# Kernel optimization log

Hardware: AMD Instinct MI355X
Metric: run time of the kernel (lower is better)

Reference implementation:

```python
import jax, jax.numpy as jnp
import numpy as np

B, S, D = 2, 2048, 2048
N_HEADS, N_KV_HEADS, HEAD_DIM = 16, 8, 128
N_REP = N_HEADS // N_KV_HEADS
EPS = 1e-6
SCALE = HEAD_DIM ** -0.5


def setup_inputs() -> dict:
    key = jax.random.key(0)
    ks = jax.random.split(key, 6)
    x = jax.random.normal(ks[0], (B, S, D), dtype=jnp.float32)
    # RoPE frequencies (Llama-style cis stored as interleaved [cos, sin])
    inv_freq = 1.0 / (1e6 ** (jnp.arange(0, HEAD_DIM, 2, dtype=jnp.float32) / HEAD_DIM))
    angles = jnp.arange(S, dtype=jnp.float32)[:, None] * inv_freq[None, :]  # [S, HEAD_DIM//2]
    freqs_cis = jnp.stack([jnp.cos(angles), jnp.sin(angles)], axis=-1)  # [S, HEAD_DIM//2, 2]
    wq = jax.random.normal(ks[1], (N_HEADS * HEAD_DIM, D), dtype=jnp.float32) * 0.02
    wk = jax.random.normal(ks[2], (N_KV_HEADS * HEAD_DIM, D), dtype=jnp.float32) * 0.02
    wv = jax.random.normal(ks[3], (N_KV_HEADS * HEAD_DIM, D), dtype=jnp.float32) * 0.02
    wo = jax.random.normal(ks[4], (D, N_HEADS * HEAD_DIM), dtype=jnp.float32) * 0.02
    q_norm_w = jnp.ones((HEAD_DIM,), dtype=jnp.float32)
    k_norm_w = jnp.ones((HEAD_DIM,), dtype=jnp.float32)
    return {"x": x, "freqs_cis": freqs_cis, "wq": wq, "wk": wk, "wv": wv,
            "wo": wo, "q_norm_w": q_norm_w, "k_norm_w": k_norm_w}


def _rmsnorm(t, w):
    var = jnp.mean(jnp.square(t), axis=-1, keepdims=True)
    return t * jax.lax.rsqrt(var + EPS) * w


def _apply_rope(t, cos, sin):
    # t: [B, S, H, HEAD_DIM]; cos/sin: [1, S, 1, HEAD_DIM//2]
    tp = t.reshape(*t.shape[:-1], HEAD_DIM // 2, 2)
    tr, ti = tp[..., 0], tp[..., 1]
    out = jnp.stack([tr * cos - ti * sin, tr * sin + ti * cos], axis=-1)
    return out.reshape(t.shape)


def reference(x, freqs_cis, wq, wk, wv, wo, q_norm_w, k_norm_w):
    bs, seqlen, _ = x.shape
    xq = (x @ wq.T).reshape(bs, seqlen, N_HEADS, HEAD_DIM)
    xk = (x @ wk.T).reshape(bs, seqlen, N_KV_HEADS, HEAD_DIM)
    xv = (x @ wv.T).reshape(bs, seqlen, N_KV_HEADS, HEAD_DIM)
    # per-head RMSNorm (Qwen3)
    xq = _rmsnorm(xq, q_norm_w)
    xk = _rmsnorm(xk, k_norm_w)
    # rotary embedding
    cos = freqs_cis[:seqlen, :, 0][None, :, None, :]
    sin = freqs_cis[:seqlen, :, 1][None, :, None, :]
    xq = _apply_rope(xq, cos, sin)
    xk = _apply_rope(xk, cos, sin)
    # GQA: repeat kv heads
    keys = jnp.repeat(xk, N_REP, axis=2)    # [B, S, N_HEADS, HEAD_DIM]
    values = jnp.repeat(xv, N_REP, axis=2)
    q = xq.transpose(0, 2, 1, 3)   # [B, H, S, D]
    k = keys.transpose(0, 2, 1, 3)
    v = values.transpose(0, 2, 1, 3)
    scores = jnp.einsum("bhqd,bhkd->bhqk", q, k) * SCALE
    causal = jnp.tril(jnp.ones((seqlen, seqlen), dtype=bool))
    scores = jnp.where(causal[None, None], scores, jnp.finfo(scores.dtype).min)
    attn = jax.nn.softmax(scores, axis=-1)
    out = jnp.einsum("bhqk,bhkd->bhqd", attn, v)
    out = out.transpose(0, 2, 1, 3).reshape(bs, seqlen, N_HEADS * HEAD_DIM)
    return out @ wo.T
```

## Files before the change

kernel.cpp:

```cpp
#include <hip/hip_runtime.h>

#define B_ 2
#define S_ 2048
#define D_ 2048
#define NH 16
#define NKV 8
#define HD 128
#define SCALE 0.08838834764831845f
#define CEXP 0.1275255f
#define RTHR 62.733f

typedef unsigned short u16;
typedef __attribute__((ext_vector_type(8))) short short8;
typedef __attribute__((ext_vector_type(4))) float f32x4;
typedef __attribute__((ext_vector_type(16))) float f32x16;
typedef __attribute__((ext_vector_type(4))) int i32x4;
typedef __attribute__((ext_vector_type(2))) int i32x2;

#define ASM_VMCNT(N) asm volatile("s_waitcnt vmcnt(" #N ")" ::: "memory")

__device__ __forceinline__ u16 f2b(float f) {
  union { float f; unsigned u; } c; c.f = f;
  unsigned u = c.u;
  return (u16)((u + 0x7fffu + ((u >> 16) & 1u)) >> 16);
}
__device__ __forceinline__ float b2f(u16 h) {
  union { unsigned u; float f; } c; c.u = ((unsigned)h) << 16;
  return c.f;
}
__device__ __forceinline__ float exp2f_fast(float x) {
  float r; asm("v_exp_f32 %0, %1" : "=v"(r) : "v"(x)); return r;
}
__device__ __forceinline__ int cvtpk(float a, float b) {
  int r; asm("v_cvt_pk_bf16_f32 %0, %1, %2" : "=v"(r) : "v"(a), "v"(b)); return r;
}
__device__ __forceinline__ void pl32swap(int& a, int& b) {
  asm volatile("v_permlane32_swap_b32 %0, %1" : "+v"(a), "+v"(b));
}

__device__ __forceinline__ void load_lds16(const u16* g, u16* l) {
  __builtin_amdgcn_global_load_lds(
      (const __attribute__((address_space(1))) unsigned int*)g,
      (__attribute__((address_space(3))) unsigned int*)l, 16, 0, 0);
}

__global__ __launch_bounds__(256) void cvt_all(const float* __restrict__ x,
                                               const float* __restrict__ wq,
                                               const float* __restrict__ wk,
                                               const float* __restrict__ wv,
                                               const float* __restrict__ wo,
                                               u16* __restrict__ xb,
                                               u16* __restrict__ wqkvb,
                                               u16* __restrict__ wob) {
  const int blk = blockIdx.x;
  const float* src; u16* dst; int base;
  if (blk < 8192)       { src = x;  dst = xb;                  base = blk; }
  else if (blk < 12288) { src = wq; dst = wqkvb;               base = blk - 8192; }
  else if (blk < 14336) { src = wk; dst = wqkvb + 2048 * 2048; base = blk - 12288; }
  else if (blk < 16384) { src = wv; dst = wqkvb + 3072 * 2048; base = blk - 14336; }
  else                  { src = wo; dst = wob;                 base = blk - 16384; }
  int i = base * 256 + threadIdx.x;
  float4 v = ((const float4*)src)[i];
  u16 o0 = f2b(v.x), o1 = f2b(v.y), o2 = f2b(v.z), o3 = f2b(v.w);
  unsigned long long packed = (unsigned long long)o0 | ((unsigned long long)o1 << 16) |
                              ((unsigned long long)o2 << 32) | ((unsigned long long)o3 << 48);
  ((unsigned long long*)dst)[i] = packed;
}

template<int OUTF32>
__global__ __launch_bounds__(256, 2) void gemm_bt2(const u16* __restrict__ A, const u16* __restrict__ Bm,
                                                   void* __restrict__ Cv, int M, int N, int K, int nbn) {
  __shared__ __align__(16) u16 As[2][128 * 64];
  __shared__ __align__(16) u16 Bs[2][128 * 64];
  const int tid = threadIdx.x;
  const int wave = tid >> 6, lane = tid & 63;
  const int nwg = gridDim.x, cpx = nwg >> 3;
  const int L = (blockIdx.x & 7) * cpx + (blockIdx.x >> 3);
  const int bm = L / nbn, bn = L % nbn;
  const int wr = wave >> 1, wc = wave & 1;
  const int r = lane & 15, hi = lane >> 4;

  f32x4 acc[4][4];
#pragma unroll
  for (int m = 0; m < 4; ++m)
#pragma unroll
    for (int n = 0; n < 4; ++n) acc[m][n] = (f32x4){0.f, 0.f, 0.f, 0.f};

  const int gslot = (lane & 7) ^ (lane >> 3);
  const int srow = lane >> 3;

  auto stage = [&](int buf, int k0) {
#pragma unroll
    for (int jj = 0; jj < 4; ++jj) {
      int j = wave * 4 + jj;
      int row = j * 8 + srow;
      load_lds16(A + (size_t)(bm * 128 + row) * K + k0 + gslot * 8, &As[buf][j * 512]);
      load_lds16(Bm + (size_t)(bn * 128 + row) * K + k0 + gslot * 8, &Bs[buf][j * 512]);
    }
  };

  const int nk = K >> 6;
  stage(0, 0);
  for (int kt = 0; kt < nk; ++kt) {
    if (kt + 1 < nk) {
      stage((kt + 1) & 1, (kt + 1) << 6);
      ASM_VMCNT(8);
    } else {
      ASM_VMCNT(0);
    }
    __builtin_amdgcn_sched_barrier(0);
    __builtin_amdgcn_s_barrier();
    __builtin_amdgcn_sched_barrier(0);
    const u16* as = As[kt & 1];
    const u16* bs = Bs[kt & 1];
#pragma unroll
    for (int kc = 0; kc < 2; ++kc) {
      short8 af[4], bfr[4];
#pragma unroll
      for (int m = 0; m < 4; ++m) {
        int row = wr * 64 + m * 16 + r;
        int slot = (hi + kc * 4) ^ (row & 7);
        af[m] = *(const short8*)&as[row * 64 + slot * 8];
      }
#pragma unroll
      for (int n = 0; n < 4; ++n) {
        int row = wc * 64 + n * 16 + r;
        int slot = (hi + kc * 4) ^ (row & 7);
        bfr[n] = *(const short8*)&bs[row * 64 + slot * 8];
      }
#pragma unroll
      for (int m = 0; m < 4; ++m)
#pragma unroll
        for (int n = 0; n < 4; ++n)
          acc[m][n] = __builtin_amdgcn_mfma_f32_16x16x32_bf16(af[m], bfr[n], acc[m][n], 0, 0, 0);
    }
    __builtin_amdgcn_sched_barrier(0);
    __builtin_amdgcn_s_barrier();
    __builtin_amdgcn_sched_barrier(0);
  }

#pragma unroll
  for (int m = 0; m < 4; ++m)
#pragma unroll
    for (int n = 0; n < 4; ++n)
#pragma unroll
      for (int r2 = 0; r2 < 4; ++r2) {
        int grow = bm * 128 + wr * 64 + m * 16 + hi * 4 + r2;
        int gcol = bn * 128 + wc * 64 + n * 16 + r;
        if (OUTF32)
          ((float*)Cv)[(size_t)grow * N + gcol] = acc[m][n][r2];
        else
          ((u16*)Cv)[(size_t)grow * N + gcol] = f2b(acc[m][n][r2]);
      }
}

__global__ __launch_bounds__(256) void rmsnorm_rope(const u16* __restrict__ qkv, const float* __restrict__ fc,
                                                    const float* __restrict__ qw, const float* __restrict__ kw,
                                                    u16* __restrict__ qr, u16* __restrict__ kr) {
  const int tid = threadIdx.x, wave = tid >> 6, lane = tid & 63;
  const int rowid = blockIdx.x * 4 + wave;
  const int token = rowid / 24;
  const int hh = rowid % 24;
  const int b = token >> 11, s = token & 2047;
  const bool isq = hh < 16;
  const int off = isq ? hh * 128 : 2048 + (hh - 16) * 128;
  const u16* src = qkv + (size_t)token * 4096 + off + lane * 2;
  unsigned pv = *(const unsigned*)src;
  float t0 = b2f((u16)(pv & 0xffffu));
  float t1 = b2f((u16)(pv >> 16));
  float ss = t0 * t0 + t1 * t1;
#pragma unroll
  for (int mm = 1; mm < 64; mm <<= 1) ss += __shfl_xor(ss, mm, 64);
  float rms = rsqrtf(ss * (1.0f / 128.0f) + 1e-6f);
  const float* nw = isq ? qw : kw;
  t0 *= rms * nw[lane * 2];
  t1 *= rms * nw[lane * 2 + 1];
  float c = fc[(s * 64 + lane) * 2], sn = fc[(s * 64 + lane) * 2 + 1];
  float o0 = t0 * c - t1 * sn;
  float o1 = t0 * sn + t1 * c;
  unsigned ov = (unsigned)f2b(o0) | ((unsigned)f2b(o1) << 16);
  if (isq)
    *(unsigned*)(qr + ((size_t)(b * 16 + hh) * 2048 + s) * 128 + lane * 2) = ov;
  else
    *(unsigned*)(kr + ((size_t)(b * 8 + hh - 16) * 2048 + s) * 128 + lane * 2) = ov;
}

__global__ __launch_bounds__(256) void v_transpose(const u16* __restrict__ qkv, u16* __restrict__ vt) {
  __shared__ __align__(16) u16 tile[64][136];
  const int blk = blockIdx.x;
  const int st = blk & 31, h = (blk >> 5) & 7, b = blk >> 8;
  const int s0 = st * 64, t = threadIdx.x;
#pragma unroll
  for (int p = 0; p < 4; ++p) {
    int row = p * 16 + (t >> 4), c8 = (t & 15) * 8;
    const u16* src = qkv + (size_t)(b * 2048 + s0 + row) * 4096 + 3072 + h * 128 + c8;
    *(short8*)&tile[row][c8] = *(const short8*)src;
  }
  __syncthreads();
  const int d = t >> 1, j0 = (t & 1) * 32;
  u16* dst = vt + ((size_t)(b * 8 + h) * 128 + d) * 2048 + s0 + j0;
#pragma unroll
  for (int j = 0; j < 32; j += 8) {
    short8 v;
#pragma unroll
    for (int u = 0; u < 8; ++u) v[u] = (short)tile[j0 + j + u][d];
    *(short8*)(dst + j) = v;
  }
}

__global__ __launch_bounds__(256, 2) void attn5(const u16* __restrict__ qr, const u16* __restrict__ kr,
                                                const u16* __restrict__ vt, u16* __restrict__ ao) {
  __shared__ __align__(16) u16 Ks[2][64 * 128];
  __shared__ __align__(16) u16 Vs[2][128 * 64];
  const int tid = threadIdx.x, wave = tid >> 6, lane = tid & 63;
  const int ql = lane & 31, lh = lane >> 5;

  const int xcd = blockIdx.x & 7, idx = blockIdx.x >> 3;
  const int bh = xcd * 4 + (idx & 3);
  const int p = idx >> 2;
  const int b = bh >> 4, h = bh & 15, hkv = h >> 1;

  const u16* Q  = qr + (size_t)(b * 16 + h) * S_ * HD;
  const u16* Kg = kr + (size_t)(b * 8 + hkv) * S_ * HD;
  const u16* Vg = vt + (size_t)(b * 8 + hkv) * HD * S_;

  auto stage = [&](int buf, int kv0) {
#pragma unroll
    for (int inst = 0; inst < 4; ++inst) {
      int pp = wave * 4096 + inst * 1024 + lane * 16;
      int row = pp >> 8;
      int colb = (pp & 255) ^ ((row & 7) << 4);
      load_lds16(Kg + (((size_t)(kv0 + row)) << 7) + (colb >> 1),
                 &Ks[buf][(wave * 4096 + inst * 1024) >> 1]);
    }
#pragma unroll
    for (int inst = 0; inst < 4; ++inst) {
      int pp = wave * 4096 + inst * 1024 + lane * 16;
      int d = pp >> 7;
      int colb = (pp & 127) ^ ((d & 7) << 4);
      load_lds16(Vg + (size_t)d * S_ + kv0 + (colb >> 1),
                 &Vs[buf][(wave * 4096 + inst * 1024) >> 1]);
    }
  };

#pragma unroll 1
  for (int half = 0; half < 2; ++half) {
    const int t = half ? p : 15 - p;
    const int q0w = t * 128 + wave * 32;
    const int nsteps = 2 * (t + 1);

    short8 qf[8];
#pragma unroll
    for (int ki = 0; ki < 8; ++ki)
      qf[ki] = *(const short8*)(Q + (size_t)(q0w + ql) * HD + ki * 16 + lh * 8);

    f32x16 o[4];
#pragma unroll
    for (int dt = 0; dt < 4; ++dt) o[dt] = 0.f;
    float m = -1e30f, l = 0.f;

    stage(0, 0);
    for (int i = 0; i < nsteps; ++i) {
      const int kv0 = i * 64;
      const u16* kb = Ks[i & 1];
      const u16* vb = Vs[i & 1];
      if (i + 1 < nsteps) {
        stage((i + 1) & 1, kv0 + 64);
        ASM_VMCNT(8);
      } else {
        ASM_VMCNT(0);
      }
      __builtin_amdgcn_sched_barrier(0);
      __builtin_amdgcn_s_barrier();
      __builtin_amdgcn_sched_barrier(0);

      if (kv0 < q0w + 32) {
        f32x16 sacc[2];
        sacc[0] = 0.f; sacc[1] = 0.f;
        __builtin_amdgcn_s_setprio(1);
#pragma unroll
        for (int ki = 0; ki < 8; ++ki) {
          const int off = ki * 32 + lh * 16;
#pragma unroll
          for (int kvt = 0; kvt < 2; ++kvt) {
            const int row = kvt * 32 + ql;
            short8 kf = *(const short8*)&kb[(row << 7) + ((off ^ ((row & 7) << 4)) >> 1)];
            sacc[kvt] = __builtin_amdgcn_mfma_f32_32x32x16_bf16(kf, qf[ki], sacc[kvt], 0, 0, 0);
          }
        }
        __builtin_amdgcn_s_setprio(0);
        const int q = q0w + ql;
        if (kv0 + 64 > q0w) {
#pragma unroll
          for (int kvt = 0; kvt < 2; ++kvt) {
            const int kvb = kv0 + kvt * 32 + 4 * lh;
#pragma unroll
            for (int reg = 0; reg < 16; ++reg) {
              const int kvr = kvb + (reg & 3) + 8 * (reg >> 2);
              sacc[kvt][reg] = (kvr > q) ? -1e30f : sacc[kvt][reg];
            }
          }
        }
        float mx = sacc[0][0];
#pragma unroll
        for (int kvt = 0; kvt < 2; ++kvt)
#pragma unroll
          for (int reg = 0; reg < 16; ++reg) mx = fmaxf(mx, sacc[kvt][reg]);
        mx = fmaxf(mx, __shfl_xor(mx, 32, 64));
        if (__any(mx > m + RTHR)) {
          float mn = fmaxf(m, mx);
          float sc = exp2f_fast((m - mn) * CEXP);
          l *= sc;
          m = mn;
#pragma unroll
          for (int dt = 0; dt < 4; ++dt)
#pragma unroll
            for (int reg = 0; reg < 16; ++reg) o[dt][reg] *= sc;
        }
        short8 pf[4];
        const float mc = m * CEXP;
        float ps = 0.f;
#pragma unroll
        for (int kvt = 0; kvt < 2; ++kvt) {
          float pv[16];
#pragma unroll
          for (int reg = 0; reg < 16; ++reg) {
            pv[reg] = exp2f_fast(__builtin_fmaf(sacc[kvt][reg], CEXP, -mc));
            ps += pv[reg];
          }
          int A0 = cvtpk(pv[0], pv[1]),  B0 = cvtpk(pv[2], pv[3]);
          int C0 = cvtpk(pv[4], pv[5]),  D0 = cvtpk(pv[6], pv[7]);
          int A1 = cvtpk(pv[8], pv[9]),  B1 = cvtpk(pv[10], pv[11]);
          int C1 = cvtpk(pv[12], pv[13]), D1 = cvtpk(pv[14], pv[15]);
          pl32swap(A0, C0);
          pl32swap(B0, D0);
          pl32swap(A1, C1);
          pl32swap(B1, D1);
          i32x4 w0 = (i32x4){A0, B0, C0, D0};
          i32x4 w1 = (i32x4){A1, B1, C1, D1};
          pf[kvt * 2]     = *(short8*)&w0;
          pf[kvt * 2 + 1] = *(short8*)&w1;
        }
        l += ps;
        __builtin_amdgcn_s_setprio(1);
#pragma unroll
        for (int kc = 0; kc < 4; ++kc) {
          const int off = kc * 32 + lh * 16;
#pragma unroll
          for (int dt = 0; dt < 4; ++dt) {
            const int d = dt * 32 + ql;
            short8 vf = *(const short8*)&vb[(d << 6) + ((off ^ ((d & 7) << 4)) >> 1)];
            o[dt] = __builtin_amdgcn_mfma_f32_32x32x16_bf16(vf, pf[kc], o[dt], 0, 0, 0);
          }
        }
        __builtin_amdgcn_s_setprio(0);
      }
      __builtin_amdgcn_sched_barrier(0);
      __builtin_amdgcn_s_barrier();
      __builtin_amdgcn_sched_barrier(0);
    }

    l += __shfl_xor(l, 32, 64);
    const float inv = 1.0f / l;
    const size_t rowoff = ((size_t)(b * 2048 + q0w + ql)) * 2048 + h * 128;
#pragma unroll
    for (int dt = 0; dt < 4; ++dt)
#pragma unroll
      for (int g = 0; g < 4; ++g) {
        const int d0 = dt * 32 + 8 * g + 4 * lh;
        int w0 = cvtpk(o[dt][4 * g] * inv, o[dt][4 * g + 1] * inv);
        int w1 = cvtpk(o[dt][4 * g + 2] * inv, o[dt][4 * g + 3] * inv);
        i32x2 pk = (i32x2){w0, w1};
        *(i32x2*)((u16*)ao + rowoff + d0) = pk;
      }
  }
}

extern "C" void kernel_launch(void* const* d_in, const int* in_sizes, int n_in,
                              void* d_out, int out_size, void* d_ws, size_t ws_size,
                              hipStream_t stream) {
  const float* x = (const float*)d_in[0];
  const float* fc = (const float*)d_in[1];
  const float* wq = (const float*)d_in[2];
  const float* wk = (const float*)d_in[3];
  const float* wv = (const float*)d_in[4];
  const float* wo = (const float*)d_in[5];
  const float* qw = (const float*)d_in[6];
  const float* kw = (const float*)d_in[7];
  float* out = (float*)d_out;
  char* ws = (char*)d_ws;

  u16* xb    = (u16*)(ws);
  u16* wqkvb = (u16*)(ws + 16777216);
  u16* wob   = (u16*)(ws + 33554432);
  u16* qkv   = (u16*)(ws + 41943040);
  u16* qrope = (u16*)(ws + 75497472);
  u16* krope = (u16*)(ws + 92274688);
  u16* vtb   = (u16*)(ws + 100663296);
  u16* ao    = (u16*)(ws + 109051904);

  cvt_all<<<20480, 256, 0, stream>>>(x, wq, wk, wv, wo, xb, wqkvb, wob);

  gemm_bt2<0><<<1024, 256, 0, stream>>>(xb, wqkvb, (void*)qkv, 4096, 4096, 2048, 32);

  rmsnorm_rope<<<24576, 256, 0, stream>>>(qkv, fc, qw, kw, qrope, krope);
  v_transpose<<<512, 256, 0, stream>>>(qkv, vtb);

  attn5<<<256, 256, 0, stream>>>(qrope, krope, vtb, ao);

  gemm_bt2<1><<<512, 256, 0, stream>>>(ao, wob, (void*)out, 4096, 2048, 2048, 16);
}
```

Measured before the change: 224.9 us.

## Use 256x256-tile 8-wave GEMM with split-K-half pipelining for QKV projection

Adds a new GEMM kernel using 256x256 output tiles with 512 threads (8 waves, each computing 128x64), staging each 64-wide K step as two 32-wide halves interleaved with MFMA phases and barriers. It is used for the QKV projection in place of the 128x128 kernel. Larger tiles raise arithmetic intensity and cut global and L2 traffic per FLOP, while the finer-grained staging overlaps loads with compute. The cost is fewer workgroups (256 over the CUs), more barriers per iteration, and higher register and LDS pressure. The barrier sequences are also factored into a macro.

```diff
diff --git a/kernel.cpp b/kernel.cpp
--- a/kernel.cpp
+++ b/kernel.cpp
@@ -18,6 +18,8 @@
 typedef __attribute__((ext_vector_type(2))) int i32x2;
 
 #define ASM_VMCNT(N) asm volatile("s_waitcnt vmcnt(" #N ")" ::: "memory")
+#define SBAR do { __builtin_amdgcn_sched_barrier(0); __builtin_amdgcn_s_barrier(); __builtin_amdgcn_sched_barrier(0); } while (0)
+#define LGKM0 do { asm volatile("s_waitcnt lgkmcnt(0)" ::: "memory"); __builtin_amdgcn_sched_barrier(0); } while (0)
 
 __device__ __forceinline__ u16 f2b(float f) {
   union { float f; unsigned u; } c; c.f = f;
@@ -67,6 +69,106 @@
   ((unsigned long long*)dst)[i] = packed;
 }
 
+#define LDA4(dst, SRC, MI0) \
+  { _Pragma("unroll") for (int i2 = 0; i2 < 4; ++i2) { \
+      const int arow = wr * 128 + (MI0 + i2) * 16 + r; \
+      dst[i2] = *(const short8*)&(SRC)[arow * 32 + ((hi ^ ((arow >> 1) & 3)) << 3)]; } }
+#define LDB4(dst, SRC) \
+  { _Pragma("unroll") for (int n2 = 0; n2 < 4; ++n2) { \
+      const int brow = wc * 64 + n2 * 16 + r; \
+      dst[n2] = *(const short8*)&(SRC)[brow * 32 + ((hi ^ ((brow >> 1) & 3)) << 3)]; } }
+#define MFMA16(MI0, AF, BF) \
+  { __builtin_amdgcn_s_setprio(1); \
+    _Pragma("unroll") for (int i2 = 0; i2 < 4; ++i2) \
+    _Pragma("unroll") for (int n2 = 0; n2 < 4; ++n2) \
+      acc[MI0 + i2][n2] = __builtin_amdgcn_mfma_f32_16x16x32_bf16(AF[i2], BF[n2], acc[MI0 + i2][n2], 0, 0, 0); \
+    __builtin_amdgcn_s_setprio(0); }
+
+template<int OUTF32>
+__global__ __launch_bounds__(512, 2) void gemm256(const u16* __restrict__ A, const u16* __restrict__ Bm,
+                                                  void* __restrict__ Cv, int M, int N, int K, int nbn) {
+  __shared__ __align__(16) u16 As[2][2][8192];
+  __shared__ __align__(16) u16 Bs[2][2][8192];
+  const int tid = threadIdx.x;
+  const int wave = tid >> 6, lane = tid & 63;
+  const int cpx = gridDim.x >> 3;
+  const int L = (blockIdx.x & 7) * cpx + (blockIdx.x >> 3);
+  const int bm = L / nbn, bn = L % nbn;
+  const int wr = wave >> 2, wc = wave & 3;
+  const int r = lane & 15, hi = lane >> 4;
+  const int rowA0 = bm * 256, rowB0 = bn * 256;
+
+  f32x4 acc[8][4];
+#pragma unroll
+  for (int mi = 0; mi < 8; ++mi)
+#pragma unroll
+    for (int ni = 0; ni < 4; ++ni) acc[mi][ni] = (f32x4){0.f, 0.f, 0.f, 0.f};
+
+  auto stage_half = [&](const u16* G, int rowbase, u16* ldsb, int kcol) {
+#pragma unroll
+    for (int l = 0; l < 2; ++l) {
+      const int p = wave * 2048 + l * 1024 + lane * 16;
+      const int row = p >> 6, slot = (p >> 4) & 3;
+      const int kg = slot ^ ((row >> 1) & 3);
+      load_lds16(G + (size_t)(rowbase + row) * K + kcol + kg * 8,
+                 ldsb + ((wave * 2048 + l * 1024) >> 1));
+    }
+  };
+
+  stage_half(A,  rowA0, &As[0][0][0], 0);
+  stage_half(Bm, rowB0, &Bs[0][0][0], 0);
+  stage_half(A,  rowA0, &As[0][1][0], 32);
+  stage_half(Bm, rowB0, &Bs[0][1][0], 32);
+  ASM_VMCNT(4);
+  __builtin_amdgcn_s_barrier();
+
+  const int nk = K >> 6;
+  for (int kt = 0; kt < nk; ++kt) {
+    const int c = kt & 1, nb2 = c ^ 1;
+    const int kn = (kt + 1) << 6;
+    const bool hn = kt + 1 < nk;
+    const u16* a0 = As[c][0]; const u16* b0 = Bs[c][0];
+    const u16* a1 = As[c][1]; const u16* b1 = Bs[c][1];
+    short8 af[4], bf[4];
+    LDB4(bf, b0); LDA4(af, a0, 0);
+    if (hn) stage_half(A, rowA0, &As[nb2][0][0], kn);
+    SBAR; LGKM0;
+    MFMA16(0, af, bf);
+    SBAR;
+    LDA4(af, a0, 4);
+    if (hn) stage_half(Bm, rowB0, &Bs[nb2][0][0], kn);
+    ASM_VMCNT(4);
+    SBAR; LGKM0;
+    MFMA16(4, af, bf);
+    SBAR;
+    LDB4(bf, b1); LDA4(af, a1, 0);
+    if (hn) stage_half(A, rowA0, &As[nb2][1][0], kn + 32);
+    SBAR; LGKM0;
+    MFMA16(0, af, bf);
+    SBAR;
+    LDA4(af, a1, 4);
+    if (hn) stage_half(Bm, rowB0, &Bs[nb2][1][0], kn + 32);
+    ASM_VMCNT(4);
+    SBAR; LGKM0;
+    MFMA16(4, af, bf);
+    SBAR;
+  }
+
+#pragma unroll
+  for (int mi = 0; mi < 8; ++mi)
+#pragma unroll
+    for (int ni = 0; ni < 4; ++ni)
+#pragma unroll
+      for (int r2 = 0; r2 < 4; ++r2) {
+        int grow = bm * 256 + wr * 128 + mi * 16 + hi * 4 + r2;
+        int gcol = bn * 256 + wc * 64 + ni * 16 + r;
+        if (OUTF32)
+          ((float*)Cv)[(size_t)grow * N + gcol] = acc[mi][ni][r2];
+        else
+          ((u16*)Cv)[(size_t)grow * N + gcol] = f2b(acc[mi][ni][r2]);
+      }
+}
+
 template<int OUTF32>
 __global__ __launch_bounds__(256, 2) void gemm_bt2(const u16* __restrict__ A, const u16* __restrict__ Bm,
                                                    void* __restrict__ Cv, int M, int N, int K, int nbn) {
@@ -108,9 +210,7 @@
     } else {
       ASM_VMCNT(0);
     }
-    __builtin_amdgcn_sched_barrier(0);
-    __builtin_amdgcn_s_barrier();
-    __builtin_amdgcn_sched_barrier(0);
+    SBAR;
     const u16* as = As[kt & 1];
     const u16* bs = Bs[kt & 1];
 #pragma unroll
@@ -134,9 +234,7 @@
         for (int n = 0; n < 4; ++n)
           acc[m][n] = __builtin_amdgcn_mfma_f32_16x16x32_bf16(af[m], bfr[n], acc[m][n], 0, 0, 0);
     }
-    __builtin_amdgcn_sched_barrier(0);
-    __builtin_amdgcn_s_barrier();
-    __builtin_amdgcn_sched_barrier(0);
+    SBAR;
   }
 
 #pragma unroll
@@ -270,9 +368,7 @@
       } else {
         ASM_VMCNT(0);
       }
-      __builtin_amdgcn_sched_barrier(0);
-      __builtin_amdgcn_s_barrier();
-      __builtin_amdgcn_sched_barrier(0);
+      SBAR;
 
       if (kv0 < q0w + 32) {
         f32x16 sacc[2];
@@ -355,9 +451,7 @@
         }
         __builtin_amdgcn_s_setprio(0);
       }
-      __builtin_amdgcn_sched_barrier(0);
-      __builtin_amdgcn_s_barrier();
-      __builtin_amdgcn_sched_barrier(0);
+      SBAR;
     }
 
     l += __shfl_xor(l, 32, 64);
@@ -401,7 +495,7 @@
 
   cvt_all<<<20480, 256, 0, stream>>>(x, wq, wk, wv, wo, xb, wqkvb, wob);
 
-  gemm_bt2<0><<<1024, 256, 0, stream>>>(xb, wqkvb, (void*)qkv, 4096, 4096, 2048, 32);
+  gemm256<0><<<256, 512, 0, stream>>>(xb, wqkvb, (void*)qkv, 4096, 4096, 2048, 16);
 
   rmsnorm_rope<<<24576, 256, 0, stream>>>(qkv, fc, qw, kw, qrope, krope);
   v_transpose<<<512, 256, 0, stream>>>(qkv, vtb);
```

New measurement: 217.0 us. 3.5% less time.
